# Optimization experiments

Measured on AMD Instinct MI355X. Metric: run time of the kernel, lower is better.

The kernel has to match this reference:

```python
import jax, jax.numpy as jnp
import numpy as np

B, H, T, OUT, MLP_H = 4096, 1024, 60, 2, 64
IN = H + 4

def setup_inputs() -> dict:
    key = jax.random.key(0)
    ks = jax.random.split(key, 12)
    s = 1.0 / np.sqrt(H)
    return {
        "z": jax.random.normal(ks[0], (B, H), jnp.float32),
        "last_vel": jax.random.normal(ks[1], (B, 2), jnp.float32),
        "last_pos": jax.random.normal(ks[2], (B, 2), jnp.float32),
        "W_ih": jax.random.uniform(ks[3], (4 * H, IN), jnp.float32, -s, s),
        "W_hh": jax.random.uniform(ks[4], (4 * H, H), jnp.float32, -s, s),
        "b_ih": jax.random.uniform(ks[5], (4 * H,), jnp.float32, -s, s),
        "b_hh": jax.random.uniform(ks[6], (4 * H,), jnp.float32, -s, s),
        "W1": jax.random.uniform(ks[7], (MLP_H, H), jnp.float32, -s, s),
        "b1": jax.random.uniform(ks[8], (MLP_H,), jnp.float32, -s, s),
        "W2": jax.random.uniform(ks[9], (OUT, MLP_H), jnp.float32, -s, s),
        "b2": jax.random.uniform(ks[10], (OUT,), jnp.float32, -s, s),
    }

def _forward(z, last_vel, last_pos, W_ih, W_hh, b_ih, b_hh, W1, b1, W2, b2):
    z_aug = jnp.concatenate([z, last_pos, last_vel], axis=-1)  # (B, H+4)
    # input is identical at every timestep -> precompute input projection once
    x_gates = z_aug @ W_ih.T + b_ih + b_hh  # (B, 4H)

    def step(carry, _):
        h, c = carry
        gates = x_gates + h @ W_hh.T  # (B, 4H)
        i, f, g, o = jnp.split(gates, 4, axis=-1)  # torch gate order i,f,g,o
        i = jax.nn.sigmoid(i)
        f = jax.nn.sigmoid(f)
        g = jnp.tanh(g)
        o = jax.nn.sigmoid(o)
        c = f * c + i * g
        h = o * jnp.tanh(c)
        return (h, c), h

    h0 = jnp.zeros((z.shape[0], W_hh.shape[1]), z.dtype)
    _, hs = jax.lax.scan(step, (h0, h0), None, length=T)  # (T, B, H)
    out = jnp.transpose(hs, (1, 0, 2))  # (B, T, H)
    delta = jax.nn.relu(out @ W1.T + b1) @ W2.T + b2  # (B, T, 2)
    return jnp.cumsum(delta, axis=1) + last_pos[:, None, :]

def reference(z, last_vel, last_pos, W_ih, W_hh, b_ih, b_hh, W1, b1, W2, b2):
    return _forward(z, last_vel, last_pos, W_ih, W_hh, b_ih, b_hh, W1, b1, W2, b2)
```

## Files before the change

kernel.cpp:

```cpp
#include <hip/hip_runtime.h>
#include <stdint.h>

#define B_    4096
#define H_    1024
#define T_    60
#define IN_   1028
#define KA_   1056
#define G4_   4096
#define MLPH_ 64
#define NB_   6

typedef __attribute__((ext_vector_type(8))) short bf16x8;
typedef __attribute__((ext_vector_type(4))) float f32x4;
typedef __attribute__((ext_vector_type(4))) unsigned short u16x4;

#define GLOBAL_AS __attribute__((address_space(1)))
#define LDS_AS    __attribute__((address_space(3)))

__device__ __forceinline__ void gload_lds16(const void* g, void* l) {
  __builtin_amdgcn_global_load_lds((GLOBAL_AS void*)const_cast<void*>(g),
                                   (LDS_AS void*)l, 16, 0, 0);
}

__device__ __forceinline__ unsigned short f2bf(float f) {
  union { float f; unsigned int u; } v; v.f = f;
  unsigned int r = v.u + 0x7FFFu + ((v.u >> 16) & 1u);
  return (unsigned short)(r >> 16);
}

__device__ __forceinline__ float bf2f(unsigned short u) {
  union { unsigned int u; float f; } v; v.u = ((unsigned int)u) << 16;
  return v.f;
}

__device__ __forceinline__ float sigmf(float x) {
  float e = __expf(-x);
  return __builtin_amdgcn_rcpf(1.0f + e);
}

__device__ __forceinline__ float tanh_fast(float x) {
  x = fminf(fmaxf(x, -15.0f), 15.0f);
  float e = __expf(2.0f * x);
  return (e - 1.0f) * __builtin_amdgcn_rcpf(e + 1.0f);
}


__global__ void k_conv_bf16(const float* __restrict__ src,
                            unsigned short* __restrict__ dst, int n) {
  int i = blockIdx.x * blockDim.x + threadIdx.x;
  int stride = gridDim.x * blockDim.x;
  for (; i < n; i += stride) dst[i] = f2bf(src[i]);
}

__global__ void k_conv_wih(const float* __restrict__ w,
                           unsigned short* __restrict__ dst) {
  int i = blockIdx.x * blockDim.x + threadIdx.x;
  int stride = gridDim.x * blockDim.x;
  const int n = G4_ * KA_;
  for (; i < n; i += stride) {
    int r = i / KA_, k = i - r * KA_;
    dst[i] = (k < IN_) ? f2bf(w[(size_t)r * IN_ + k]) : (unsigned short)0;
  }
}

__global__ void k_build_zaug(const float* __restrict__ z,
                             const float* __restrict__ lp,
                             const float* __restrict__ lv,
                             unsigned short* __restrict__ dst) {
  int i = blockIdx.x * blockDim.x + threadIdx.x;
  int stride = gridDim.x * blockDim.x;
  const int n = B_ * KA_;
  for (; i < n; i += stride) {
    int b = i / KA_, k = i - b * KA_;
    float v;
    if (k < H_)            v = z[(size_t)b * H_ + k];
    else if (k < H_ + 2)   v = lp[b * 2 + (k - H_)];
    else if (k < IN_)      v = lv[b * 2 + (k - H_ - 2)];
    else                   v = 0.0f;
    dst[i] = f2bf(v);
  }
}



__global__ __launch_bounds__(256, 4) void k_xgates(
    const unsigned short* __restrict__ zaug, const unsigned short* __restrict__ wih,
    const float* __restrict__ bih, const float* __restrict__ bhh,
    u16x4* __restrict__ xg4) {
  __shared__ unsigned short As[2][128 * 32];
  __shared__ unsigned short Bs[2][128 * 32];
  const int tid = threadIdx.x, lane = tid & 63, wave = tid >> 6;
  const int bx = blockIdx.x, by = blockIdx.y;
  const int wm = wave >> 1, wn = wave & 1;
  const int rs = lane >> 2;
  const int c16 = (((lane & 3) ^ ((lane >> 3) & 3))) * 16;
  const int rdslot = ((lane >> 4) ^ ((lane >> 1) & 3)) * 8;

  const char* asrc0 = (const char*)zaug + ((size_t)(bx * 128 + (wave * 2 + 0) * 16 + rs) * KA_) * 2 + c16;
  const char* asrc1 = (const char*)zaug + ((size_t)(bx * 128 + (wave * 2 + 1) * 16 + rs) * KA_) * 2 + c16;
  const char* bsrc0 = (const char*)wih  + ((size_t)(wave * H_ + by * 32 +  0 + rs) * KA_) * 2 + c16;
  const char* bsrc1 = (const char*)wih  + ((size_t)(wave * H_ + by * 32 + 16 + rs) * KA_) * 2 + c16;

  f32x4 acc[4][4];
#pragma unroll
  for (int g = 0; g < 4; ++g)
#pragma unroll
    for (int m = 0; m < 4; ++m) acc[g][m] = {0.f, 0.f, 0.f, 0.f};

  gload_lds16(asrc0, &As[0][(wave * 2 + 0) * 512]);
  gload_lds16(asrc1, &As[0][(wave * 2 + 1) * 512]);
  gload_lds16(bsrc0, &Bs[0][(wave * 2 + 0) * 512]);
  gload_lds16(bsrc1, &Bs[0][(wave * 2 + 1) * 512]);
  __syncthreads();

  const int nt = KA_ / 32;
  int cur = 0;
  for (int kk = 0; kk < nt; ++kk) {
    if (kk + 1 < nt) {
      const size_t kb = (size_t)(kk + 1) * 64;
      gload_lds16(asrc0 + kb, &As[cur ^ 1][(wave * 2 + 0) * 512]);
      gload_lds16(asrc1 + kb, &As[cur ^ 1][(wave * 2 + 1) * 512]);
      gload_lds16(bsrc0 + kb, &Bs[cur ^ 1][(wave * 2 + 0) * 512]);
      gload_lds16(bsrc1 + kb, &Bs[cur ^ 1][(wave * 2 + 1) * 512]);
    }
    bf16x8 a[4], b[4];
#pragma unroll
    for (int m = 0; m < 4; ++m)
      a[m] = *(const bf16x8*)&As[cur][(wm * 64 + m * 16 + (lane & 15)) * 32 + rdslot];
#pragma unroll
    for (int g = 0; g < 4; ++g)
      b[g] = *(const bf16x8*)&Bs[cur][((g * 2 + wn) * 16 + (lane & 15)) * 32 + rdslot];
#pragma unroll
    for (int g = 0; g < 4; ++g)
#pragma unroll
      for (int m = 0; m < 4; ++m)
        acc[g][m] = __builtin_amdgcn_mfma_f32_16x16x32_bf16(a[m], b[g], acc[g][m], 0, 0, 0);
    __syncthreads();
    cur ^= 1;
  }

  const int r0 = (lane >> 4) * 4, cl = lane & 15;
  const int hc = by * 32 + wn * 16 + cl;
  const float bi = bih[hc]        + bhh[hc];
  const float bf = bih[1024 + hc] + bhh[1024 + hc];
  const float bg = bih[2048 + hc] + bhh[2048 + hc];
  const float bo = bih[3072 + hc] + bhh[3072 + hc];
#pragma unroll
  for (int m = 0; m < 4; ++m)
#pragma unroll
    for (int j = 0; j < 4; ++j) {
      int row = bx * 128 + wm * 64 + m * 16 + r0 + j;
      u16x4 st = {f2bf(acc[0][m][j] + bi), f2bf(acc[1][m][j] + bf),
                  f2bf(acc[2][m][j] + bg), f2bf(acc[3][m][j] + bo)};
      xg4[(size_t)row * H_ + hc] = st;
    }
}


__global__ __launch_bounds__(256, 4) void k_step(
    const unsigned short* __restrict__ hprev, const unsigned short* __restrict__ whh,
    const u16x4* __restrict__ xg4, float* __restrict__ cbuf,
    unsigned short* __restrict__ hout) {
  __shared__ unsigned short As[2][128 * 32];
  __shared__ unsigned short Bs[2][128 * 32];
  const int tid = threadIdx.x, lane = tid & 63, wave = tid >> 6;
  const int bx = blockIdx.x, by = blockIdx.y;
  const int wm = wave >> 1, wn = wave & 1;
  const int rs = lane >> 2;
  const int c16 = (((lane & 3) ^ ((lane >> 3) & 3))) * 16;
  const int rdslot = ((lane >> 4) ^ ((lane >> 1) & 3)) * 8;

  const char* asrc0 = (const char*)hprev + ((size_t)(bx * 128 + (wave * 2 + 0) * 16 + rs) * H_) * 2 + c16;
  const char* asrc1 = (const char*)hprev + ((size_t)(bx * 128 + (wave * 2 + 1) * 16 + rs) * H_) * 2 + c16;
  const char* bsrc0 = (const char*)whh   + ((size_t)(wave * H_ + by * 32 +  0 + rs) * H_) * 2 + c16;
  const char* bsrc1 = (const char*)whh   + ((size_t)(wave * H_ + by * 32 + 16 + rs) * H_) * 2 + c16;

  f32x4 acc[4][4];
#pragma unroll
  for (int g = 0; g < 4; ++g)
#pragma unroll
    for (int m = 0; m < 4; ++m) acc[g][m] = {0.f, 0.f, 0.f, 0.f};

  gload_lds16(asrc0, &As[0][(wave * 2 + 0) * 512]);
  gload_lds16(asrc1, &As[0][(wave * 2 + 1) * 512]);
  gload_lds16(bsrc0, &Bs[0][(wave * 2 + 0) * 512]);
  gload_lds16(bsrc1, &Bs[0][(wave * 2 + 1) * 512]);
  __syncthreads();

  const int nt = H_ / 32;
  int cur = 0;
  for (int kk = 0; kk < nt; ++kk) {
    if (kk + 1 < nt) {
      const size_t kb = (size_t)(kk + 1) * 64;
      gload_lds16(asrc0 + kb, &As[cur ^ 1][(wave * 2 + 0) * 512]);
      gload_lds16(asrc1 + kb, &As[cur ^ 1][(wave * 2 + 1) * 512]);
      gload_lds16(bsrc0 + kb, &Bs[cur ^ 1][(wave * 2 + 0) * 512]);
      gload_lds16(bsrc1 + kb, &Bs[cur ^ 1][(wave * 2 + 1) * 512]);
    }
    bf16x8 a[4], b[4];
#pragma unroll
    for (int m = 0; m < 4; ++m)
      a[m] = *(const bf16x8*)&As[cur][(wm * 64 + m * 16 + (lane & 15)) * 32 + rdslot];
#pragma unroll
    for (int g = 0; g < 4; ++g)
      b[g] = *(const bf16x8*)&Bs[cur][((g * 2 + wn) * 16 + (lane & 15)) * 32 + rdslot];
#pragma unroll
    for (int g = 0; g < 4; ++g)
#pragma unroll
      for (int m = 0; m < 4; ++m)
        acc[g][m] = __builtin_amdgcn_mfma_f32_16x16x32_bf16(a[m], b[g], acc[g][m], 0, 0, 0);
    __syncthreads();
    cur ^= 1;
  }

  const int r0 = (lane >> 4) * 4, cl = lane & 15;
  const int hc = by * 32 + wn * 16 + cl;
#pragma unroll
  for (int m = 0; m < 4; ++m)
#pragma unroll
    for (int j = 0; j < 4; ++j) {
      int row = bx * 128 + wm * 64 + m * 16 + r0 + j;
      size_t ci = (size_t)row * H_ + hc;
      u16x4 xv = xg4[ci];
      float iv = sigmf(acc[0][m][j] + bf2f(xv[0]));
      float fv = sigmf(acc[1][m][j] + bf2f(xv[1]));
      float gv = tanh_fast(acc[2][m][j] + bf2f(xv[2]));
      float ov = sigmf(acc[3][m][j] + bf2f(xv[3]));
      float cv = fv * cbuf[ci] + iv * gv;
      cbuf[ci] = cv;
      hout[ci] = f2bf(ov * tanh_fast(cv));
    }
}


__global__ __launch_bounds__(256) void k_mlp(
    const unsigned short* __restrict__ hring, const unsigned short* __restrict__ w1,
    const float* __restrict__ b1, const float* __restrict__ w2,
    const float* __restrict__ b2, float* __restrict__ delta, int t0) {
  __shared__ unsigned short As[64 * 32];
  __shared__ unsigned short Bs[64 * 32];
  __shared__ float hid[64][65];
  const int tid = threadIdx.x, lane = tid & 63, wave = tid >> 6;
  const int bx = blockIdx.x;
  const unsigned short* h = hring + (size_t)blockIdx.y * B_ * H_;
  const int t = t0 + blockIdx.y;
  const int rs = lane >> 2;
  const int c16 = (((lane & 3) ^ ((lane >> 3) & 3))) * 16;
  const int rdslot = ((lane >> 4) ^ ((lane >> 1) & 3)) * 8;

  f32x4 acc[4];
#pragma unroll
  for (int n = 0; n < 4; ++n) acc[n] = {0.f, 0.f, 0.f, 0.f};

  for (int kk = 0; kk < H_ / 32; ++kk) {
    const int k0 = kk * 32;
    __syncthreads();
    {
      int row = bx * 64 + wave * 16 + rs;
      gload_lds16((const char*)h + ((size_t)row * H_ + k0) * 2 + c16,
                  (char*)As + wave * 1024);
    }
    {
      int jj = wave * 16 + rs;
      gload_lds16((const char*)w1 + ((size_t)jj * H_ + k0) * 2 + c16,
                  (char*)Bs + wave * 1024);
    }
    __syncthreads();
    bf16x8 a = *(const bf16x8*)&As[(wave * 16 + (lane & 15)) * 32 + rdslot];
#pragma unroll
    for (int n = 0; n < 4; ++n) {
      bf16x8 b = *(const bf16x8*)&Bs[(n * 16 + (lane & 15)) * 32 + rdslot];
      acc[n] = __builtin_amdgcn_mfma_f32_16x16x32_bf16(a, b, acc[n], 0, 0, 0);
    }
  }

  const int r0 = (lane >> 4) * 4, cl = lane & 15;
#pragma unroll
  for (int n = 0; n < 4; ++n)
#pragma unroll
    for (int j = 0; j < 4; ++j) {
      int row = wave * 16 + r0 + j;
      int col = n * 16 + cl;
      hid[row][col] = fmaxf(acc[n][j] + b1[col], 0.0f);
    }
  __syncthreads();

  if (tid < 128) {
    int r = tid >> 1, d = tid & 1;
    float s = b2[d];
#pragma unroll 8
    for (int k2 = 0; k2 < 64; ++k2) s += hid[r][k2] * w2[d * 64 + k2];
    delta[((size_t)(bx * 64 + r) * T_ + t) * 2 + d] = s;
  }
}


__global__ void k_cumsum(const float* __restrict__ delta,
                         const float* __restrict__ lp, float* __restrict__ out) {
  int id = blockIdx.x * blockDim.x + threadIdx.x;
  if (id >= B_ * 2) return;
  int b = id >> 1, d = id & 1;
  float cum = lp[b * 2 + d];
  size_t base = (size_t)b * T_ * 2 + d;
  for (int t = 0; t < T_; ++t) {
    cum += delta[base + t * 2];
    out[base + t * 2] = cum;
  }
}


extern "C" void kernel_launch(void* const* d_in, const int* in_sizes, int n_in,
                              void* d_out, int out_size, void* d_ws, size_t ws_size,
                              hipStream_t stream) {
  const float* z   = (const float*)d_in[0];
  const float* lv  = (const float*)d_in[1];
  const float* lp  = (const float*)d_in[2];
  const float* Wih = (const float*)d_in[3];
  const float* Whh = (const float*)d_in[4];
  const float* bih = (const float*)d_in[5];
  const float* bhh = (const float*)d_in[6];
  const float* W1  = (const float*)d_in[7];
  const float* b1  = (const float*)d_in[8];
  const float* W2  = (const float*)d_in[9];
  const float* b2  = (const float*)d_in[10];
  float* out = (float*)d_out;

  char* ws = (char*)d_ws;
  size_t off = 0;
  u16x4*          xg4    = (u16x4*)(ws + off);          off += (size_t)B_ * H_ * 8;
  unsigned short* whh_bf = (unsigned short*)(ws + off); off += (size_t)G4_ * H_ * 2;
  unsigned short* wih_bf = (unsigned short*)(ws + off); off += (size_t)G4_ * KA_ * 2;
  unsigned short* zaug   = (unsigned short*)(ws + off); off += (size_t)B_ * KA_ * 2;
  unsigned short* w1_bf  = (unsigned short*)(ws + off); off += (size_t)MLPH_ * H_ * 2;
  unsigned short* hring  = (unsigned short*)(ws + off); off += (size_t)NB_ * B_ * H_ * 2;
  float*          cbuf   = (float*)(ws + off);          off += (size_t)B_ * H_ * 4;
  float*          delta  = (float*)(ws + off);          off += (size_t)B_ * T_ * 2 * 4;

  const size_t BH = (size_t)B_ * H_;

  hipMemsetAsync(hring + (NB_ - 1) * BH, 0, BH * 2, stream);
  hipMemsetAsync(cbuf, 0, BH * 4, stream);

  k_conv_bf16 <<<2048, 256, 0, stream>>>(Whh, whh_bf, G4_ * H_);
  k_conv_wih  <<<2048, 256, 0, stream>>>(Wih, wih_bf);
  k_build_zaug<<<2048, 256, 0, stream>>>(z, lp, lv, zaug);
  k_conv_bf16 <<<256, 256, 0, stream>>>(W1, w1_bf, MLPH_ * H_);

  k_xgates<<<dim3(32, 32), 256, 0, stream>>>(zaug, wih_bf, bih, bhh, xg4);

  for (int t = 0; t < T_; ++t) {
    const unsigned short* hp = hring + (size_t)((t + NB_ - 1) % NB_) * BH;
    unsigned short*       hc = hring + (size_t)(t % NB_) * BH;
    k_step<<<dim3(32, 32), 256, 0, stream>>>(hp, whh_bf, xg4, cbuf, hc);
    if ((t % NB_) == NB_ - 1)
      k_mlp<<<dim3(64, NB_), 256, 0, stream>>>(hring, w1_bf, b1, W2, b2, delta, t - (NB_ - 1));
  }

  k_cumsum<<<32, 256, 0, stream>>>(delta, lp, out);
}
```

Before: 3.001 ms.

## Replace per-step kernel launches with a persistent cooperative LSTM kernel

Adds a single cooperative persistent kernel with 256 blocks of 512 threads. Each block owns a 256x64 tile of the hidden state. It computes its input-gate projection once and keeps it in registers, keeps the cell state in LDS, and uses grid.sync between timesteps. The per-step MLP head is fused in after the sync, which removes the xg4 and cbuf global traffic and 60+ kernel launches. The cost is one grid barrier per step, a 128KB LDS footprint, and heavy register pressure from holding xgr and acc. If the cooperative launch fails, the code falls back to the multi-kernel path with an MLP launch per step.

New measurement: 11.20 ms. 3.73x slower.

```diff
diff --git a/kernel.cpp b/kernel.cpp
--- a/kernel.cpp
+++ b/kernel.cpp
@@ -1,5 +1,8 @@
 #include <hip/hip_runtime.h>
+#include <hip/hip_cooperative_groups.h>
 #include <stdint.h>
+
+namespace cg = cooperative_groups;
 
 #define B_    4096
 #define H_    1024
@@ -8,7 +11,6 @@
 #define KA_   1056
 #define G4_   4096
 #define MLPH_ 64
-#define NB_   6
 
 typedef __attribute__((ext_vector_type(8))) short bf16x8;
 typedef __attribute__((ext_vector_type(4))) float f32x4;
@@ -82,6 +84,160 @@
 }
 
 
+__global__ __launch_bounds__(512, 2) void k_persist(
+    const unsigned short* __restrict__ zaug, const unsigned short* __restrict__ wih,
+    const unsigned short* __restrict__ whh, const unsigned short* __restrict__ w1,
+    const float* __restrict__ bih, const float* __restrict__ bhh,
+    const float* __restrict__ b1, const float* __restrict__ w2,
+    const float* __restrict__ b2,
+    unsigned short* h_a, unsigned short* h_b,
+    float* __restrict__ delta) {
+  __shared__ char smem[131072];
+  unsigned short* As = (unsigned short*)smem;
+  unsigned short* Bs = (unsigned short*)(smem + 32768);
+  float* cS  = (float*)(smem + 65536);
+  float* hid = (float*)smem;
+
+  const int tid = threadIdx.x, lane = tid & 63, wave = tid >> 6;
+  const int wm = wave >> 2, wn = wave & 3;
+  const int cl = lane & 15, sl16 = lane >> 4;
+  const int bId = blockIdx.x;
+  const int by = (bId & 7) * 2 + ((bId >> 3) & 1);
+  const int bx = bId >> 4;
+
+  const int q = tid >> 2;
+  const int s16   = ((tid & 3) ^ ((tid >> 3) & 3)) * 16;
+  const int slot8 = (sl16 ^ ((cl >> 1) & 3)) * 8;
+  const int hcl = wn * 16 + cl;
+  const int hc  = by * 64 + hcl;
+
+  for (int i = tid; i < 16384; i += 512) cS[i] = 0.0f;
+
+  float bias[4];
+#pragma unroll
+  for (int g = 0; g < 4; ++g) bias[g] = bih[g * H_ + hc] + bhh[g * H_ + hc];
+
+  f32x4 acc[4][8];
+  bf16x8 afr[4], bfr[4];
+
+  auto gemm = [&](const char* asrc, size_t astr, const char* bsrc, size_t bstr, int nt) {
+    const char* ap  = asrc + (size_t)(bx * 256 + q) * astr + s16;
+    const char* bp0 = bsrc + (size_t)((q >> 6) * H_ + by * 64 + (q & 63)) * bstr + s16;
+    const char* bp1 = bsrc + (size_t)((2 + (q >> 6)) * H_ + by * 64 + (q & 63)) * bstr + s16;
+    auto stage = [&](int kt, int bs) {
+      gload_lds16(ap + (size_t)kt * 64,              (char*)As + bs * 16384 + tid * 16);
+      gload_lds16(ap + 128 * astr + (size_t)kt * 64, (char*)As + bs * 16384 + 8192 + tid * 16);
+      gload_lds16(bp0 + (size_t)kt * 64,             (char*)Bs + bs * 16384 + tid * 16);
+      gload_lds16(bp1 + (size_t)kt * 64,             (char*)Bs + bs * 16384 + 8192 + tid * 16);
+    };
+    stage(0, 0);
+    __syncthreads();
+    for (int kt = 0; kt < nt; ++kt) {
+      const int cur = kt & 1;
+      if (kt + 1 < nt) stage(kt + 1, cur ^ 1);
+      const unsigned short* Ab = As + cur * 8192;
+      const unsigned short* Bb = Bs + cur * 8192;
+#pragma unroll
+      for (int g = 0; g < 4; ++g)
+        bfr[g] = *(const bf16x8*)&Bb[(g * 64 + hcl) * 32 + slot8];
+#pragma unroll
+      for (int m = 0; m < 4; ++m)
+        afr[m] = *(const bf16x8*)&Ab[(wm * 128 + m * 16 + cl) * 32 + slot8];
+#pragma unroll
+      for (int g = 0; g < 4; ++g)
+#pragma unroll
+        for (int m = 0; m < 4; ++m)
+          acc[g][m] = __builtin_amdgcn_mfma_f32_16x16x32_bf16(afr[m], bfr[g], acc[g][m], 0, 0, 0);
+#pragma unroll
+      for (int m = 0; m < 4; ++m)
+        afr[m] = *(const bf16x8*)&Ab[(wm * 128 + (4 + m) * 16 + cl) * 32 + slot8];
+#pragma unroll
+      for (int g = 0; g < 4; ++g)
+#pragma unroll
+        for (int m = 0; m < 4; ++m)
+          acc[g][4 + m] = __builtin_amdgcn_mfma_f32_16x16x32_bf16(afr[m], bfr[g], acc[g][4 + m], 0, 0, 0);
+      __syncthreads();
+    }
+  };
+
+#pragma unroll
+  for (int g = 0; g < 4; ++g)
+#pragma unroll
+    for (int m = 0; m < 8; ++m) acc[g][m] = {0.f, 0.f, 0.f, 0.f};
+  gemm((const char*)zaug, (size_t)KA_ * 2, (const char*)wih, (size_t)KA_ * 2, KA_ / 32);
+
+  u16x4 xgr[8][4];
+#pragma unroll
+  for (int m = 0; m < 8; ++m)
+#pragma unroll
+    for (int j = 0; j < 4; ++j)
+      xgr[m][j] = u16x4{f2bf(acc[0][m][j] + bias[0]), f2bf(acc[1][m][j] + bias[1]),
+                        f2bf(acc[2][m][j] + bias[2]), f2bf(acc[3][m][j] + bias[3])};
+
+  cg::grid_group grid = cg::this_grid();
+
+  for (int t = 0; t < T_; ++t) {
+    const unsigned short* hp = (t & 1) ? h_b : h_a;
+    unsigned short*       hw = (t & 1) ? h_a : h_b;
+
+#pragma unroll
+    for (int g = 0; g < 4; ++g)
+#pragma unroll
+      for (int m = 0; m < 8; ++m) acc[g][m] = {0.f, 0.f, 0.f, 0.f};
+    gemm((const char*)hp, (size_t)H_ * 2, (const char*)whh, (size_t)H_ * 2, H_ / 32);
+
+#pragma unroll
+    for (int m = 0; m < 8; ++m)
+#pragma unroll
+      for (int j = 0; j < 4; ++j) {
+        int erowl = wm * 128 + m * 16 + sl16 * 4 + j;
+        int cidx  = erowl * 64 + (hcl ^ ((erowl & 7) << 3));
+        u16x4 xv = xgr[m][j];
+        float iv = sigmf(acc[0][m][j] + bf2f(xv[0]));
+        float fv = sigmf(acc[1][m][j] + bf2f(xv[1]));
+        float gv = tanh_fast(acc[2][m][j] + bf2f(xv[2]));
+        float ov = sigmf(acc[3][m][j] + bf2f(xv[3]));
+        float cv = fv * cS[cidx] + iv * gv;
+        cS[cidx] = cv;
+        hw[(size_t)(bx * 256 + erowl) * H_ + hc] = f2bf(ov * tanh_fast(cv));
+      }
+
+    __threadfence();
+    grid.sync();
+    __threadfence();
+
+    {
+      f32x4 macc = {0.f, 0.f, 0.f, 0.f};
+      const char* ha = (const char*)hw + (size_t)(bId * 16 + cl) * 2048 + sl16 * 16;
+      const char* wb = (const char*)w1 + (size_t)((wave & 3) * 16 + cl) * 2048 + sl16 * 16;
+      if (wave < 4) {
+#pragma unroll 8
+        for (int kt = 0; kt < H_ / 32; ++kt) {
+          bf16x8 av = *(const bf16x8*)(ha + (size_t)kt * 64);
+          bf16x8 bv = *(const bf16x8*)(wb + (size_t)kt * 64);
+          macc = __builtin_amdgcn_mfma_f32_16x16x32_bf16(av, bv, macc, 0, 0, 0);
+        }
+      }
+      __syncthreads();
+      if (wave < 4) {
+        float b1v = b1[wave * 16 + cl];
+#pragma unroll
+        for (int j = 0; j < 4; ++j)
+          hid[(sl16 * 4 + j) * 64 + wave * 16 + cl] = fmaxf(macc[j] + b1v, 0.0f);
+      }
+      __syncthreads();
+      if (tid < 32) {
+        int r = tid >> 1, d = tid & 1;
+        float s = b2[d];
+#pragma unroll 16
+        for (int k = 0; k < 64; ++k) s += hid[r * 64 + k] * w2[d * 64 + k];
+        delta[((size_t)(bId * 16 + r) * T_ + t) * 2 + d] = s;
+      }
+      __syncthreads();
+    }
+  }
+}
+
 
 __global__ __launch_bounds__(256, 4) void k_xgates(
     const unsigned short* __restrict__ zaug, const unsigned short* __restrict__ wih,
@@ -156,7 +312,6 @@
     }
 }
 
-
 __global__ __launch_bounds__(256, 4) void k_step(
     const unsigned short* __restrict__ hprev, const unsigned short* __restrict__ whh,
     const u16x4* __restrict__ xg4, float* __restrict__ cbuf,
@@ -232,18 +387,15 @@
     }
 }
 
-
 __global__ __launch_bounds__(256) void k_mlp(
-    const unsigned short* __restrict__ hring, const unsigned short* __restrict__ w1,
+    const unsigned short* __restrict__ h, const unsigned short* __restrict__ w1,
     const float* __restrict__ b1, const float* __restrict__ w2,
-    const float* __restrict__ b2, float* __restrict__ delta, int t0) {
+    const float* __restrict__ b2, float* __restrict__ delta, int t) {
   __shared__ unsigned short As[64 * 32];
   __shared__ unsigned short Bs[64 * 32];
   __shared__ float hid[64][65];
   const int tid = threadIdx.x, lane = tid & 63, wave = tid >> 6;
   const int bx = blockIdx.x;
-  const unsigned short* h = hring + (size_t)blockIdx.y * B_ * H_;
-  const int t = t0 + blockIdx.y;
   const int rs = lane >> 2;
   const int c16 = (((lane & 3) ^ ((lane >> 3) & 3))) * 16;
   const int rdslot = ((lane >> 4) ^ ((lane >> 1) & 3)) * 8;
@@ -327,33 +479,40 @@
 
   char* ws = (char*)d_ws;
   size_t off = 0;
+  unsigned short* zaug   = (unsigned short*)(ws + off); off += (size_t)B_ * KA_ * 2;
+  unsigned short* wih_bf = (unsigned short*)(ws + off); off += (size_t)G4_ * KA_ * 2;
+  unsigned short* whh_bf = (unsigned short*)(ws + off); off += (size_t)G4_ * H_ * 2;
+  unsigned short* w1_bf  = (unsigned short*)(ws + off); off += (size_t)MLPH_ * H_ * 2;
+  unsigned short* h_a    = (unsigned short*)(ws + off); off += (size_t)B_ * H_ * 2;
+  unsigned short* h_b    = (unsigned short*)(ws + off); off += (size_t)B_ * H_ * 2;
+  float*          delta  = (float*)(ws + off);          off += (size_t)B_ * T_ * 2 * 4;
   u16x4*          xg4    = (u16x4*)(ws + off);          off += (size_t)B_ * H_ * 8;
-  unsigned short* whh_bf = (unsigned short*)(ws + off); off += (size_t)G4_ * H_ * 2;
-  unsigned short* wih_bf = (unsigned short*)(ws + off); off += (size_t)G4_ * KA_ * 2;
-  unsigned short* zaug   = (unsigned short*)(ws + off); off += (size_t)B_ * KA_ * 2;
-  unsigned short* w1_bf  = (unsigned short*)(ws + off); off += (size_t)MLPH_ * H_ * 2;
-  unsigned short* hring  = (unsigned short*)(ws + off); off += (size_t)NB_ * B_ * H_ * 2;
   float*          cbuf   = (float*)(ws + off);          off += (size_t)B_ * H_ * 4;
-  float*          delta  = (float*)(ws + off);          off += (size_t)B_ * T_ * 2 * 4;
 
   const size_t BH = (size_t)B_ * H_;
-
-  hipMemsetAsync(hring + (NB_ - 1) * BH, 0, BH * 2, stream);
-  hipMemsetAsync(cbuf, 0, BH * 4, stream);
+  hipMemsetAsync(h_a, 0, BH * 2, stream);
 
   k_conv_bf16 <<<2048, 256, 0, stream>>>(Whh, whh_bf, G4_ * H_);
   k_conv_wih  <<<2048, 256, 0, stream>>>(Wih, wih_bf);
   k_build_zaug<<<2048, 256, 0, stream>>>(z, lp, lv, zaug);
   k_conv_bf16 <<<256, 256, 0, stream>>>(W1, w1_bf, MLPH_ * H_);
 
-  k_xgates<<<dim3(32, 32), 256, 0, stream>>>(zaug, wih_bf, bih, bhh, xg4);
-
-  for (int t = 0; t < T_; ++t) {
-    const unsigned short* hp = hring + (size_t)((t + NB_ - 1) % NB_) * BH;
-    unsigned short*       hc = hring + (size_t)(t % NB_) * BH;
-    k_step<<<dim3(32, 32), 256, 0, stream>>>(hp, whh_bf, xg4, cbuf, hc);
-    if ((t % NB_) == NB_ - 1)
-      k_mlp<<<dim3(64, NB_), 256, 0, stream>>>(hring, w1_bf, b1, W2, b2, delta, t - (NB_ - 1));
+  void* kargs[] = {
+    (void*)&zaug, (void*)&wih_bf, (void*)&whh_bf, (void*)&w1_bf,
+    (void*)&bih, (void*)&bhh, (void*)&b1, (void*)&W2, (void*)&b2,
+    (void*)&h_a, (void*)&h_b, (void*)&delta
+  };
+  hipError_t cerr = hipLaunchCooperativeKernel((const void*)k_persist, dim3(256),
+                                               dim3(512), kargs, 0, stream);
+  if (cerr != hipSuccess) {
+    hipMemsetAsync(cbuf, 0, BH * 4, stream);
+    k_xgates<<<dim3(32, 32), 256, 0, stream>>>(zaug, wih_bf, bih, bhh, xg4);
+    for (int t = 0; t < T_; ++t) {
+      const unsigned short* hp = (t & 1) ? h_b : h_a;
+      unsigned short*       hc = (t & 1) ? h_a : h_b;
+      k_step<<<dim3(32, 32), 256, 0, stream>>>(hp, whh_bf, xg4, cbuf, hc);
+      k_mlp <<<64, 256, 0, stream>>>(hc, w1_bf, b1, W2, b2, delta, t);
+    }
   }
 
   k_cumsum<<<32, 256, 0, stream>>>(delta, lp, out);
```

## Widen LSTM step tile to 64 hidden columns and remap blocks for L2 locality

Applied to the files above, without the earlier changes.

Each step block now computes 128 batch rows by 64 hidden columns across all four gates, doubling the B tile and the accumulator count per wave. The grid becomes 1D with 512 blocks, and a block-id remapping interleaves hidden-column tiles so that neighbouring blocks share W_hh and h slices in cache. The aim is more MFMA work per A-tile load and fewer total A reloads. The cost is higher register and LDS use, which lowers occupancy (launch bounds drop from 4 to 2) and leaves only 512 blocks to fill the GPU.

Result: slower. 3.482 ms (+16.0%).

```diff
diff --git a/kernel.cpp b/kernel.cpp
--- a/kernel.cpp
+++ b/kernel.cpp
@@ -157,78 +157,96 @@
 }
 
 
-__global__ __launch_bounds__(256, 4) void k_step(
+__global__ __launch_bounds__(256, 2) void k_step(
     const unsigned short* __restrict__ hprev, const unsigned short* __restrict__ whh,
     const u16x4* __restrict__ xg4, float* __restrict__ cbuf,
     unsigned short* __restrict__ hout) {
   __shared__ unsigned short As[2][128 * 32];
-  __shared__ unsigned short Bs[2][128 * 32];
+  __shared__ unsigned short Bs[2][256 * 32];
   const int tid = threadIdx.x, lane = tid & 63, wave = tid >> 6;
-  const int bx = blockIdx.x, by = blockIdx.y;
+  const int id = blockIdx.x;
+  const int sl = id >> 3;
+  const int by = (id & 7) * 2 + (sl & 1);
+  const int bx = sl >> 1;
   const int wm = wave >> 1, wn = wave & 1;
   const int rs = lane >> 2;
-  const int c16 = (((lane & 3) ^ ((lane >> 3) & 3))) * 16;
+  const int cl = lane & 15;
+  const int c16 = ((lane & 3) ^ ((lane >> 3) & 3)) * 16;
   const int rdslot = ((lane >> 4) ^ ((lane >> 1) & 3)) * 8;
 
-  const char* asrc0 = (const char*)hprev + ((size_t)(bx * 128 + (wave * 2 + 0) * 16 + rs) * H_) * 2 + c16;
-  const char* asrc1 = (const char*)hprev + ((size_t)(bx * 128 + (wave * 2 + 1) * 16 + rs) * H_) * 2 + c16;
-  const char* bsrc0 = (const char*)whh   + ((size_t)(wave * H_ + by * 32 +  0 + rs) * H_) * 2 + c16;
-  const char* bsrc1 = (const char*)whh   + ((size_t)(wave * H_ + by * 32 + 16 + rs) * H_) * 2 + c16;
-
-  f32x4 acc[4][4];
+  const char* a0 = (const char*)hprev + ((size_t)(bx * 128 + (wave * 2 + 0) * 16 + rs) * H_) * 2 + c16;
+  const char* a1 = (const char*)hprev + ((size_t)(bx * 128 + (wave * 2 + 1) * 16 + rs) * H_) * 2 + c16;
+  const char* bsrc[4];
+#pragma unroll
+  for (int i = 0; i < 4; ++i) {
+    int ch = wave * 4 + i;
+    int row = (ch >> 2) * H_ + by * 64 + (ch & 3) * 16 + rs;
+    bsrc[i] = (const char*)whh + (size_t)row * (H_ * 2) + c16;
+  }
+
+  auto stage = [&](int kt, int bu) {
+    const size_t kb = (size_t)kt * 64;
+    gload_lds16(a0 + kb, &As[bu][(wave * 2 + 0) * 512]);
+    gload_lds16(a1 + kb, &As[bu][(wave * 2 + 1) * 512]);
+#pragma unroll
+    for (int i = 0; i < 4; ++i)
+      gload_lds16(bsrc[i] + kb, &Bs[bu][(wave * 4 + i) * 512]);
+  };
+
+  f32x4 acc[4][2][4];
 #pragma unroll
   for (int g = 0; g < 4; ++g)
 #pragma unroll
-    for (int m = 0; m < 4; ++m) acc[g][m] = {0.f, 0.f, 0.f, 0.f};
-
-  gload_lds16(asrc0, &As[0][(wave * 2 + 0) * 512]);
-  gload_lds16(asrc1, &As[0][(wave * 2 + 1) * 512]);
-  gload_lds16(bsrc0, &Bs[0][(wave * 2 + 0) * 512]);
-  gload_lds16(bsrc1, &Bs[0][(wave * 2 + 1) * 512]);
+    for (int n = 0; n < 2; ++n)
+#pragma unroll
+      for (int m = 0; m < 4; ++m) acc[g][n][m] = {0.f, 0.f, 0.f, 0.f};
+
+  stage(0, 0);
   __syncthreads();
 
   const int nt = H_ / 32;
-  int cur = 0;
   for (int kk = 0; kk < nt; ++kk) {
-    if (kk + 1 < nt) {
-      const size_t kb = (size_t)(kk + 1) * 64;
-      gload_lds16(asrc0 + kb, &As[cur ^ 1][(wave * 2 + 0) * 512]);
-      gload_lds16(asrc1 + kb, &As[cur ^ 1][(wave * 2 + 1) * 512]);
-      gload_lds16(bsrc0 + kb, &Bs[cur ^ 1][(wave * 2 + 0) * 512]);
-      gload_lds16(bsrc1 + kb, &Bs[cur ^ 1][(wave * 2 + 1) * 512]);
-    }
+    const int cur = kk & 1;
+    if (kk + 1 < nt) stage(kk + 1, cur ^ 1);
+    const unsigned short* Ab = As[cur];
+    const unsigned short* Bb = Bs[cur];
     bf16x8 a[4], b[4];
 #pragma unroll
     for (int m = 0; m < 4; ++m)
-      a[m] = *(const bf16x8*)&As[cur][(wm * 64 + m * 16 + (lane & 15)) * 32 + rdslot];
-#pragma unroll
-    for (int g = 0; g < 4; ++g)
-      b[g] = *(const bf16x8*)&Bs[cur][((g * 2 + wn) * 16 + (lane & 15)) * 32 + rdslot];
-#pragma unroll
-    for (int g = 0; g < 4; ++g)
-#pragma unroll
-      for (int m = 0; m < 4; ++m)
-        acc[g][m] = __builtin_amdgcn_mfma_f32_16x16x32_bf16(a[m], b[g], acc[g][m], 0, 0, 0);
+      a[m] = *(const bf16x8*)&Ab[(wm * 64 + m * 16 + cl) * 32 + rdslot];
+#pragma unroll
+    for (int n = 0; n < 2; ++n) {
+#pragma unroll
+      for (int g = 0; g < 4; ++g)
+        b[g] = *(const bf16x8*)&Bb[(g * 64 + wn * 32 + n * 16 + cl) * 32 + rdslot];
+#pragma unroll
+      for (int g = 0; g < 4; ++g)
+#pragma unroll
+        for (int m = 0; m < 4; ++m)
+          acc[g][n][m] = __builtin_amdgcn_mfma_f32_16x16x32_bf16(a[m], b[g], acc[g][n][m], 0, 0, 0);
+    }
     __syncthreads();
-    cur ^= 1;
-  }
-
-  const int r0 = (lane >> 4) * 4, cl = lane & 15;
-  const int hc = by * 32 + wn * 16 + cl;
+  }
+
+  const int r0 = (lane >> 4) * 4;
 #pragma unroll
   for (int m = 0; m < 4; ++m)
 #pragma unroll
     for (int j = 0; j < 4; ++j) {
       int row = bx * 128 + wm * 64 + m * 16 + r0 + j;
-      size_t ci = (size_t)row * H_ + hc;
-      u16x4 xv = xg4[ci];
-      float iv = sigmf(acc[0][m][j] + bf2f(xv[0]));
-      float fv = sigmf(acc[1][m][j] + bf2f(xv[1]));
-      float gv = tanh_fast(acc[2][m][j] + bf2f(xv[2]));
-      float ov = sigmf(acc[3][m][j] + bf2f(xv[3]));
-      float cv = fv * cbuf[ci] + iv * gv;
-      cbuf[ci] = cv;
-      hout[ci] = f2bf(ov * tanh_fast(cv));
+#pragma unroll
+      for (int n = 0; n < 2; ++n) {
+        int hc = by * 64 + wn * 32 + n * 16 + cl;
+        size_t ci = (size_t)row * H_ + hc;
+        u16x4 xv = xg4[ci];
+        float iv = sigmf(acc[0][n][m][j] + bf2f(xv[0]));
+        float fv = sigmf(acc[1][n][m][j] + bf2f(xv[1]));
+        float gv = tanh_fast(acc[2][n][m][j] + bf2f(xv[2]));
+        float ov = sigmf(acc[3][n][m][j] + bf2f(xv[3]));
+        float cv = fv * cbuf[ci] + iv * gv;
+        cbuf[ci] = cv;
+        hout[ci] = f2bf(ov * tanh_fast(cv));
+      }
     }
 }
 
@@ -351,7 +369,7 @@
   for (int t = 0; t < T_; ++t) {
     const unsigned short* hp = hring + (size_t)((t + NB_ - 1) % NB_) * BH;
     unsigned short*       hc = hring + (size_t)(t % NB_) * BH;
-    k_step<<<dim3(32, 32), 256, 0, stream>>>(hp, whh_bf, xg4, cbuf, hc);
+    k_step<<<512, 256, 0, stream>>>(hp, whh_bf, xg4, cbuf, hc);
     if ((t % NB_) == NB_ - 1)
       k_mlp<<<dim3(64, NB_), 256, 0, stream>>>(hring, w1_bf, b1, W2, b2, delta, t - (NB_ - 1));
   }
```

## Triple-buffer LDS tiles in LSTM step GEMM with explicit vmcnt waits

Applied to the files above, without the earlier changes.

Converts the recurrent step kernel's double-buffered global-to-LDS pipeline into a three-stage ring, prefetching two K-tiles ahead. Fine-grained s_waitcnt vmcnt counts and raw s_barrier replace __syncthreads, so only the oldest tile's loads are waited on. The goal is to hide global load latency in a memory-latency-bound per-timestep GEMM. In exchange, LDS use rises and the occupancy hint drops from 4 to 3 blocks per CU. Correctness also now depends on vmcnt counting being exact, and it is unclear whether LDS writes from global_load_lds are visible after the barrier without an lgkm wait.

New measurement: 3.394 ms. +13.1%, slower.

```diff
diff --git a/kernel.cpp b/kernel.cpp
--- a/kernel.cpp
+++ b/kernel.cpp
@@ -157,12 +157,12 @@
 }
 
 
-__global__ __launch_bounds__(256, 4) void k_step(
+__global__ __launch_bounds__(256, 3) void k_step(
     const unsigned short* __restrict__ hprev, const unsigned short* __restrict__ whh,
     const u16x4* __restrict__ xg4, float* __restrict__ cbuf,
     unsigned short* __restrict__ hout) {
-  __shared__ unsigned short As[2][128 * 32];
-  __shared__ unsigned short Bs[2][128 * 32];
+  __shared__ unsigned short As[3][128 * 32];
+  __shared__ unsigned short Bs[3][128 * 32];
   const int tid = threadIdx.x, lane = tid & 63, wave = tid >> 6;
   const int bx = blockIdx.x, by = blockIdx.y;
   const int wm = wave >> 1, wn = wave & 1;
@@ -181,22 +181,31 @@
 #pragma unroll
     for (int m = 0; m < 4; ++m) acc[g][m] = {0.f, 0.f, 0.f, 0.f};
 
-  gload_lds16(asrc0, &As[0][(wave * 2 + 0) * 512]);
-  gload_lds16(asrc1, &As[0][(wave * 2 + 1) * 512]);
-  gload_lds16(bsrc0, &Bs[0][(wave * 2 + 0) * 512]);
-  gload_lds16(bsrc1, &Bs[0][(wave * 2 + 1) * 512]);
-  __syncthreads();
+  auto stage = [&](int kt, int bu) {
+    const size_t kb = (size_t)kt * 64;
+    gload_lds16(asrc0 + kb, &As[bu][(wave * 2 + 0) * 512]);
+    gload_lds16(asrc1 + kb, &As[bu][(wave * 2 + 1) * 512]);
+    gload_lds16(bsrc0 + kb, &Bs[bu][(wave * 2 + 0) * 512]);
+    gload_lds16(bsrc1 + kb, &Bs[bu][(wave * 2 + 1) * 512]);
+  };
+
+  stage(0, 0);
+  stage(1, 1);
 
   const int nt = H_ / 32;
   int cur = 0;
   for (int kk = 0; kk < nt; ++kk) {
-    if (kk + 1 < nt) {
-      const size_t kb = (size_t)(kk + 1) * 64;
-      gload_lds16(asrc0 + kb, &As[cur ^ 1][(wave * 2 + 0) * 512]);
-      gload_lds16(asrc1 + kb, &As[cur ^ 1][(wave * 2 + 1) * 512]);
-      gload_lds16(bsrc0 + kb, &Bs[cur ^ 1][(wave * 2 + 0) * 512]);
-      gload_lds16(bsrc1 + kb, &Bs[cur ^ 1][(wave * 2 + 1) * 512]);
-    }
+    if (kk + 2 < nt) {
+      int nb = cur + 2; if (nb >= 3) nb -= 3;
+      stage(kk + 2, nb);
+      asm volatile("s_waitcnt vmcnt(8)" ::: "memory");
+    } else if (kk + 1 < nt) {
+      asm volatile("s_waitcnt vmcnt(4)" ::: "memory");
+    } else {
+      asm volatile("s_waitcnt vmcnt(0)" ::: "memory");
+    }
+    __builtin_amdgcn_s_barrier();
+
     bf16x8 a[4], b[4];
 #pragma unroll
     for (int m = 0; m < 4; ++m)
@@ -209,8 +218,9 @@
 #pragma unroll
       for (int m = 0; m < 4; ++m)
         acc[g][m] = __builtin_amdgcn_mfma_f32_16x16x32_bf16(a[m], b[g], acc[g][m], 0, 0, 0);
-    __syncthreads();
-    cur ^= 1;
+
+    __builtin_amdgcn_s_barrier();
+    ++cur; if (cur == 3) cur = 0;
   }
 
   const int r0 = (lane >> 4) * 4, cl = lane & 15;
```
